# Kernel tuning notes

Hardware: AMD Instinct MI355X
Metric: run time of the kernel (lower is better)

## Reference

```python
import jax, jax.numpy as jnp
import numpy as np

T, B, D = 2048, 16, 1024


def setup_inputs() -> dict:
    key = jax.random.key(0)
    ks = jax.random.split(key, 8)
    std = 1.0 / D ** 0.5
    x = jax.random.normal(ks[0], (T, B, D), dtype=jnp.float32)
    h0 = jnp.zeros((B, D), dtype=jnp.float32)
    Wx = jax.random.uniform(ks[1], (D, D), jnp.float32, -std, std)
    R = jax.random.uniform(ks[2], (D, D), jnp.float32, -std, std)
    bias = jnp.zeros((D,), dtype=jnp.float32)
    W_delta = jax.random.uniform(ks[3], (D, D), jnp.float32, -std * 0.1, std * 0.1)
    b_delta = jnp.full((D,), 3.0, dtype=jnp.float32)  # delta_init
    A = jax.random.uniform(ks[4], (D,), jnp.float32, -0.5, 0.5)  # A_init_range
    W_gate_x = jax.random.uniform(ks[5], (D, D), jnp.float32, -std, std)
    W_gate_h = jax.random.uniform(ks[6], (D, D), jnp.float32, -std, std)
    b_gate = jnp.zeros((D,), dtype=jnp.float32)
    return {"x": x, "h0": h0, "Wx": Wx, "R": R, "bias": bias,
            "W_delta": W_delta, "b_delta": b_delta, "A": A,
            "W_gate_x": W_gate_x, "W_gate_h": W_gate_h, "b_gate": b_gate}


def reference(x, h0, Wx, R, bias, W_delta, b_delta, A, W_gate_x, W_gate_h, b_gate):
    # Input-dependent timestep: dt = softplus(x @ W_delta^T + b_delta), [T,B,D]
    dt = jax.nn.softplus(jnp.einsum('tbd,ed->tbe', x, W_delta) + b_delta)
    # Mamba-style log parameterization: decay_rate in (0,1), alpha in (0,1)
    decay_rate = jnp.exp(-jnp.exp(A))                 # [D]
    alpha = jnp.exp(-dt * decay_rate)                 # [T,B,D]
    # Precompute input projection once (big GEMM outside the scan)
    wx = jnp.einsum('tbd,ed->tbe', x, Wx) + bias      # [T,B,D]

    def step(h, inp):
        wx_t, a_t = inp                               # [B,D], [B,D]
        cand = jnp.tanh(h @ R.T + wx_t)               # nonlinear candidate
        h_new = a_t * h + (1.0 - a_t) * cand          # exponential blend
        return h_new, h_new

    _, h_out = jax.lax.scan(step, h0, (wx, alpha))    # h_out: [T,B,D] == h[1:]

    # h+x selective output gate
    gate_raw = (jnp.einsum('tbd,ed->tbe', x, W_gate_x)
                + jnp.einsum('tbd,ed->tbe', h_out, W_gate_h) + b_gate)
    return h_out * jax.nn.silu(gate_raw)
```

## Files before the change

### kernel.cpp

```cpp
#include <hip/hip_runtime.h>
#include <cstdint>
#include <cstddef>

typedef _Float16 f16;
typedef _Float16 f16x8 __attribute__((ext_vector_type(8)));
typedef _Float16 f16x4v __attribute__((ext_vector_type(4)));
typedef float f32x4 __attribute__((ext_vector_type(4)));
typedef unsigned uint2v __attribute__((ext_vector_type(2)));

#define TT 2048
#define BB 16
#define DD 1024
#define MM (TT*BB)
#define LDST 40
#define FPAD 16

__global__ void cvt_kernel(const float* __restrict__ in, f16* __restrict__ out, int n4){
  int stride = gridDim.x * blockDim.x;
  for (int j = blockIdx.x*blockDim.x + threadIdx.x; j < n4; j += stride){
    float4 v = ((const float4*)in)[j];
    f16x4v o;
    o[0]=(f16)v.x; o[1]=(f16)v.y; o[2]=(f16)v.z; o[3]=(f16)v.w;
    ((f16x4v*)out)[j] = o;
  }
}

__global__ void init_rec_kernel(const float* __restrict__ h0, f16* __restrict__ hbuf,
                                unsigned* __restrict__ flags){
  int tid = blockIdx.x*blockDim.x + threadIdx.x;
  if (tid < 64*FPAD) flags[tid] = 0u;
  if (tid < BB*DD) hbuf[tid] = (f16)h0[tid];
}

__global__ __launch_bounds__(256)
void gemm_f16_kernel(const f16* __restrict__ A, const f16* __restrict__ Bw,
                     float* __restrict__ out32, f16* __restrict__ out16,
                     const float* __restrict__ vec1, const float* __restrict__ vec2,
                     const f16* __restrict__ gxin, int epi)
{
  __shared__ f16 As[128*LDST];
  __shared__ f16 Bs[128*LDST];
  const int K = DD;
  int tid = threadIdx.x;
  int l = tid & 63, w = tid >> 6;
  int wr = w >> 1, wc = w & 1;
  int bm = blockIdx.x, bn = blockIdx.y;

  f32x4 acc[4][4];
  #pragma unroll
  for (int i=0;i<4;++i)
    #pragma unroll
    for (int j=0;j<4;++j)
      acc[i][j] = (f32x4){0.f,0.f,0.f,0.f};

  const int r0 = tid >> 2;
  const int q  = tid & 3;

  for (int kt = 0; kt < K/32; ++kt){
    __syncthreads();
    #pragma unroll
    for (int hh=0; hh<2; ++hh){
      int row = hh*64 + r0;
      uint4 va = *(const uint4*)(A  + (size_t)(bm*128+row)*K + kt*32 + q*8);
      uint4 vb = *(const uint4*)(Bw + (size_t)(bn*128+row)*K + kt*32 + q*8);
      *(uint4*)(As + row*LDST + q*8) = va;
      *(uint4*)(Bs + row*LDST + q*8) = vb;
    }
    __syncthreads();
    int lr = l & 15, kg = (l >> 4) * 8;
    f16x8 af[4], bf[4];
    #pragma unroll
    for (int i=0;i<4;++i){
      af[i] = *(const f16x8*)(As + (wr*64 + i*16 + lr)*LDST + kg);
      bf[i] = *(const f16x8*)(Bs + (wc*64 + i*16 + lr)*LDST + kg);
    }
    #pragma unroll
    for (int i=0;i<4;++i)
      #pragma unroll
      for (int j=0;j<4;++j)
        acc[i][j] = __builtin_amdgcn_mfma_f32_16x16x32_f16(af[i], bf[j], acc[i][j], 0,0,0);
  }

  int lr = l & 15, lh = l >> 4;
  #pragma unroll
  for (int i=0;i<4;++i){
    #pragma unroll
    for (int j=0;j<4;++j){
      #pragma unroll
      for (int r=0;r<4;++r){
        int row = bm*128 + wr*64 + i*16 + lh*4 + r;
        int col = bn*128 + wc*64 + j*16 + lr;
        float v = acc[i][j][r];
        size_t off = (size_t)row*DD + col;
        if (epi == 0){
          out32[off] = v + vec1[col];
        } else if (epi == 1){
          float pre = v + vec1[col];
          float sp  = (pre > 20.f) ? pre : log1pf(expf(pre));
          float decay = expf(-expf(vec2[col]));
          out32[off] = expf(-sp*decay);
        } else if (epi == 2){
          out16[off] = (f16)(v + vec1[col]);
        } else {
          float g = v + (float)gxin[off];
          float hval = (float)A[off];
          out32[off] = hval * g / (1.f + expf(-g));
        }
      }
    }
  }
}

__global__ __launch_bounds__(256)
void rec_kernel(const f16* __restrict__ Rf, const float* __restrict__ wx,
                const float* __restrict__ alpha, const float* __restrict__ h0,
                f16* __restrict__ hbuf, f16* __restrict__ hout,
                unsigned* __restrict__ flags)
{
  __shared__ f16  Rlds[32*64*8];
  __shared__ float plds[3*64*4];

  int tid = threadIdx.x;
  int l = tid & 63, w = tid >> 6;
  int j = blockIdx.x;
  int e0 = j * 16;

  for (int it=0; it<8; ++it){
    int c = it*256 + tid;
    int lane = c & 63, kt = c >> 6;
    int e = e0 + (lane & 15);
    int d = kt*32 + (lane >> 4)*8;
    uint4 v = *(const uint4*)(Rf + (size_t)e*DD + d);
    *(uint4*)(Rlds + (size_t)c*8) = v;
  }

  int b = l & 15, rr0 = (l >> 4) * 4;
  float4 hstate = {0.f,0.f,0.f,0.f};
  if (w == 0)
    hstate = *(const float4*)(h0 + (size_t)b*DD + e0 + rr0);
  __syncthreads();

  for (int t = 0; t < TT; ++t){
    f32x4 wxv, alv;
    size_t off4 = ((size_t)t*BB + b)*DD + e0 + rr0;
    if (w == 0){
      if (t > 0){
        const unsigned* fp = flags + l*FPAD;
        int guard = 0;
        unsigned long long notready = 1ull;
        while (notready && guard < 1000000){
          unsigned fv = __hip_atomic_load(fp, __ATOMIC_RELAXED, __HIP_MEMORY_SCOPE_AGENT);
          notready = __ballot(fv < (unsigned)t);
          ++guard;
          if (notready) __builtin_amdgcn_s_sleep(1);
        }
      }
      wxv = *(const f32x4*)(wx + off4);
      alv = *(const f32x4*)(alpha + off4);
    } else {
      wxv = (f32x4){0,0,0,0};
      alv = (f32x4){0,0,0,0};
    }
    __syncthreads();

    const f16* hb = hbuf + (size_t)(t & 1) * (BB*DD);
    f16x8 bfrag[8];
    #pragma unroll
    for (int kk=0; kk<8; ++kk){
      int kt = w*8 + kk;
      const f16* hp = hb + (size_t)(l & 15)*DD + kt*32 + ((l >> 4)*8);
      asm volatile("global_load_dwordx4 %0, %1, off sc0 sc1"
                   : "=v"(bfrag[kk]) : "v"(hp) : "memory");
    }
    asm volatile("s_waitcnt vmcnt(0)" ::: "memory");
    __builtin_amdgcn_sched_barrier(0);

    f32x4 acc = (f32x4){0.f,0.f,0.f,0.f};
    #pragma unroll
    for (int kk=0; kk<8; ++kk){
      int kt = w*8 + kk;
      f16x8 a = *(const f16x8*)(Rlds + ((size_t)kt*64 + l)*8);
      acc = __builtin_amdgcn_mfma_f32_16x16x32_f16(a, bfrag[kk], acc, 0, 0, 0);
    }
    if (w) *(f32x4*)(plds + ((size_t)(w-1)*64 + l)*4) = acc;
    __syncthreads();

    if (w == 0){
      f32x4 v = acc;
      #pragma unroll
      for (int q=0;q<3;++q)
        v += *(const f32x4*)(plds + ((size_t)q*64 + l)*4);

      f16x4v h4;
      float hs[4] = {hstate.x, hstate.y, hstate.z, hstate.w};
      #pragma unroll
      for (int r=0;r<4;++r){
        float z = v[r] + wxv[r];
        float cand = tanhf(z);
        float hn = alv[r]*hs[r] + (1.f - alv[r])*cand;
        hs[r] = hn;
        h4[r] = (f16)hn;
      }
      hstate = (float4){hs[0], hs[1], hs[2], hs[3]};

      f16* hw = hbuf + (size_t)((t+1) & 1) * (BB*DD) + (size_t)b*DD + e0 + rr0;
      uint2v hv = __builtin_bit_cast(uint2v, h4);
      asm volatile("global_store_dwordx2 %0, %1, off sc0 sc1"
                   :: "v"(hw), "v"(hv) : "memory");
      asm volatile("s_waitcnt vmcnt(0)" ::: "memory");
      if (l == 0)
        __hip_atomic_store(flags + j*FPAD, (unsigned)(t+1),
                           __ATOMIC_RELAXED, __HIP_MEMORY_SCOPE_AGENT);
      *(f16x4v*)(hout + off4) = h4;
    }
  }
}

extern "C" void kernel_launch(void* const* d_in, const int* in_sizes, int n_in,
                              void* d_out, int out_size, void* d_ws, size_t ws_size,
                              hipStream_t stream)
{
  const float* x    = (const float*)d_in[0];
  const float* h0   = (const float*)d_in[1];
  const float* Wx   = (const float*)d_in[2];
  const float* R    = (const float*)d_in[3];
  const float* bias = (const float*)d_in[4];
  const float* Wd   = (const float*)d_in[5];
  const float* bd   = (const float*)d_in[6];
  const float* Aar  = (const float*)d_in[7];
  const float* Wgx  = (const float*)d_in[8];
  const float* Wgh  = (const float*)d_in[9];
  const float* bg   = (const float*)d_in[10];
  float* out = (float*)d_out;

  char* ws = (char*)d_ws;
  size_t off = 0;
  auto carve = [&](size_t bytes) -> void* {
    void* p = ws + off;
    off += (bytes + 255) & ~(size_t)255;
    return p;
  };
  f16* x16    = (f16*)carve((size_t)MM*DD*2);
  f16* Wx16   = (f16*)carve((size_t)DD*DD*2);
  f16* Wd16   = (f16*)carve((size_t)DD*DD*2);
  f16* Wgx16  = (f16*)carve((size_t)DD*DD*2);
  f16* Wgh16  = (f16*)carve((size_t)DD*DD*2);
  f16* R16    = (f16*)carve((size_t)DD*DD*2);
  float* alphaB = (float*)carve((size_t)MM*DD*4);
  f16* gx16   = (f16*)carve((size_t)MM*DD*2);
  f16* hout16 = (f16*)carve((size_t)MM*DD*2);
  f16* hbuf   = (f16*)carve((size_t)2*BB*DD*2);
  unsigned* flags = (unsigned*)carve(64*FPAD*4);
  if (off > ws_size) return;

  float* wxbuf = out;

  cvt_kernel<<<1024, 256, 0, stream>>>(x,   x16,   MM*DD/4);
  cvt_kernel<<<256,  256, 0, stream>>>(Wx,  Wx16,  DD*DD/4);
  cvt_kernel<<<256,  256, 0, stream>>>(Wd,  Wd16,  DD*DD/4);
  cvt_kernel<<<256,  256, 0, stream>>>(Wgx, Wgx16, DD*DD/4);
  cvt_kernel<<<256,  256, 0, stream>>>(Wgh, Wgh16, DD*DD/4);
  cvt_kernel<<<256,  256, 0, stream>>>(R,   R16,   DD*DD/4);
  init_rec_kernel<<<64, 256, 0, stream>>>(h0, hbuf, flags);

  dim3 gg(MM/128, DD/128);
  gemm_f16_kernel<<<gg, 256, 0, stream>>>(x16, Wx16,  wxbuf,  nullptr, bias, nullptr, nullptr, 0);
  gemm_f16_kernel<<<gg, 256, 0, stream>>>(x16, Wd16,  alphaB, nullptr, bd,   Aar,     nullptr, 1);
  gemm_f16_kernel<<<gg, 256, 0, stream>>>(x16, Wgx16, nullptr, gx16,   bg,   nullptr, nullptr, 2);

  rec_kernel<<<64, 256, 0, stream>>>(R16, wxbuf, alphaB, h0, hbuf, hout16, flags);

  gemm_f16_kernel<<<gg, 256, 0, stream>>>(hout16, Wgh16, out, nullptr, nullptr, nullptr, gx16, 3);
}
```

Baseline: 8.055 ms.

## Replace flag-based inter-block sync with sequence-tagged hidden-state records

The recurrent kernel previously had one wavefront spin on per-block flags, then do a block barrier, then all waves load the hidden state. Now every wave polls the hidden-state data directly. Each 4-element f16 chunk is packed into a 16-byte record that carries its timestep tag, and a wave retries its loads until all tags match. This removes the separate store-wait-then-flag-store handshake and the pre-load barrier on the serial critical path. In exchange, the hidden-state traffic per step doubles, and correctness depends on each 16-byte store landing atomically.

```diff
diff --git a/kernel.cpp b/kernel.cpp
--- a/kernel.cpp
+++ b/kernel.cpp
@@ -7,13 +7,14 @@
 typedef _Float16 f16x4v __attribute__((ext_vector_type(4)));
 typedef float f32x4 __attribute__((ext_vector_type(4)));
 typedef unsigned uint2v __attribute__((ext_vector_type(2)));
+typedef unsigned uint4v __attribute__((ext_vector_type(4)));
 
 #define TT 2048
 #define BB 16
 #define DD 1024
 #define MM (TT*BB)
 #define LDST 40
-#define FPAD 16
+#define NREC (BB*DD/4)
 
 __global__ void cvt_kernel(const float* __restrict__ in, f16* __restrict__ out, int n4){
   int stride = gridDim.x * blockDim.x;
@@ -25,11 +26,17 @@
   }
 }
 
-__global__ void init_rec_kernel(const float* __restrict__ h0, f16* __restrict__ hbuf,
-                                unsigned* __restrict__ flags){
+__global__ void init_rec_kernel(const float* __restrict__ h0, uint4v* __restrict__ recs){
   int tid = blockIdx.x*blockDim.x + threadIdx.x;
-  if (tid < 64*FPAD) flags[tid] = 0u;
-  if (tid < BB*DD) hbuf[tid] = (f16)h0[tid];
+  if (tid < NREC){
+    int b = tid >> 8, c = tid & 255;
+    float4 v = *(const float4*)(h0 + (size_t)b*DD + c*4);
+    f16x4v h4;
+    h4[0]=(f16)v.x; h4[1]=(f16)v.y; h4[2]=(f16)v.z; h4[3]=(f16)v.w;
+    uint2v hb = __builtin_bit_cast(uint2v, h4);
+    uint4v rec = {hb[0], hb[1], 0u, 0u};
+    recs[tid] = rec;
+  }
 }
 
 __global__ __launch_bounds__(256)
@@ -114,8 +121,7 @@
 __global__ __launch_bounds__(256)
 void rec_kernel(const f16* __restrict__ Rf, const float* __restrict__ wx,
                 const float* __restrict__ alpha, const float* __restrict__ h0,
-                f16* __restrict__ hbuf, f16* __restrict__ hout,
-                unsigned* __restrict__ flags)
+                uint4v* __restrict__ recs, f16* __restrict__ hout)
 {
   __shared__ f16  Rlds[32*64*8];
   __shared__ float plds[3*64*4];
@@ -138,49 +144,50 @@
   float4 hstate = {0.f,0.f,0.f,0.f};
   if (w == 0)
     hstate = *(const float4*)(h0 + (size_t)b*DD + e0 + rr0);
+
+  const int cbase = (l & 15)*256 + (l >> 4)*2;
   __syncthreads();
 
   for (int t = 0; t < TT; ++t){
-    f32x4 wxv, alv;
+    const uint4v* rb = recs + (size_t)(t & 1) * NREC;
+    unsigned expect = (unsigned)t;
+
+    uint4v r0[8], r1[8];
+    int ok = 0;
+    for (int it = 0; it < 200000 && !ok; ++it){
+      if (it) __builtin_amdgcn_s_sleep(1);
+      #pragma unroll
+      for (int kk=0; kk<8; ++kk){
+        const uint4v* p = rb + cbase + (w*8 + kk)*8;
+        asm volatile("global_load_dwordx4 %0, %1, off sc0 sc1"
+                     : "=v"(r0[kk]) : "v"(p) : "memory");
+        asm volatile("global_load_dwordx4 %0, %1, off sc0 sc1"
+                     : "=v"(r1[kk]) : "v"(p+1) : "memory");
+      }
+      asm volatile("s_waitcnt vmcnt(0)" ::: "memory");
+      __builtin_amdgcn_sched_barrier(0);
+      unsigned bad = 0;
+      #pragma unroll
+      for (int kk=0; kk<8; ++kk)
+        bad |= (r0[kk][2] ^ expect) | (r1[kk][2] ^ expect);
+      ok = (__ballot(bad != 0) == 0ull);
+    }
+
+    f32x4 wxv = (f32x4){0,0,0,0}, alv = (f32x4){0,0,0,0};
     size_t off4 = ((size_t)t*BB + b)*DD + e0 + rr0;
     if (w == 0){
-      if (t > 0){
-        const unsigned* fp = flags + l*FPAD;
-        int guard = 0;
-        unsigned long long notready = 1ull;
-        while (notready && guard < 1000000){
-          unsigned fv = __hip_atomic_load(fp, __ATOMIC_RELAXED, __HIP_MEMORY_SCOPE_AGENT);
-          notready = __ballot(fv < (unsigned)t);
-          ++guard;
-          if (notready) __builtin_amdgcn_s_sleep(1);
-        }
-      }
       wxv = *(const f32x4*)(wx + off4);
       alv = *(const f32x4*)(alpha + off4);
-    } else {
-      wxv = (f32x4){0,0,0,0};
-      alv = (f32x4){0,0,0,0};
-    }
-    __syncthreads();
-
-    const f16* hb = hbuf + (size_t)(t & 1) * (BB*DD);
-    f16x8 bfrag[8];
+    }
+
+    f32x4 acc = (f32x4){0.f,0.f,0.f,0.f};
     #pragma unroll
     for (int kk=0; kk<8; ++kk){
       int kt = w*8 + kk;
-      const f16* hp = hb + (size_t)(l & 15)*DD + kt*32 + ((l >> 4)*8);
-      asm volatile("global_load_dwordx4 %0, %1, off sc0 sc1"
-                   : "=v"(bfrag[kk]) : "v"(hp) : "memory");
-    }
-    asm volatile("s_waitcnt vmcnt(0)" ::: "memory");
-    __builtin_amdgcn_sched_barrier(0);
-
-    f32x4 acc = (f32x4){0.f,0.f,0.f,0.f};
-    #pragma unroll
-    for (int kk=0; kk<8; ++kk){
-      int kt = w*8 + kk;
+      uint4v packed = {r0[kk][0], r0[kk][1], r1[kk][0], r1[kk][1]};
+      f16x8 bfrag = __builtin_bit_cast(f16x8, packed);
       f16x8 a = *(const f16x8*)(Rlds + ((size_t)kt*64 + l)*8);
-      acc = __builtin_amdgcn_mfma_f32_16x16x32_f16(a, bfrag[kk], acc, 0, 0, 0);
+      acc = __builtin_amdgcn_mfma_f32_16x16x32_f16(a, bfrag, acc, 0, 0, 0);
     }
     if (w) *(f32x4*)(plds + ((size_t)(w-1)*64 + l)*4) = acc;
     __syncthreads();
@@ -203,14 +210,11 @@
       }
       hstate = (float4){hs[0], hs[1], hs[2], hs[3]};
 
-      f16* hw = hbuf + (size_t)((t+1) & 1) * (BB*DD) + (size_t)b*DD + e0 + rr0;
-      uint2v hv = __builtin_bit_cast(uint2v, h4);
-      asm volatile("global_store_dwordx2 %0, %1, off sc0 sc1"
-                   :: "v"(hw), "v"(hv) : "memory");
-      asm volatile("s_waitcnt vmcnt(0)" ::: "memory");
-      if (l == 0)
-        __hip_atomic_store(flags + j*FPAD, (unsigned)(t+1),
-                           __ATOMIC_RELAXED, __HIP_MEMORY_SCOPE_AGENT);
+      uint2v hb = __builtin_bit_cast(uint2v, h4);
+      uint4v rec = {hb[0], hb[1], (unsigned)(t+1), 0u};
+      uint4v* rp = recs + (size_t)((t+1) & 1)*NREC + (size_t)b*256 + (e0 + rr0)/4;
+      asm volatile("global_store_dwordx4 %0, %1, off sc0 sc1"
+                   :: "v"(rp), "v"(rec) : "memory");
       *(f16x4v*)(hout + off4) = h4;
     }
   }
@@ -249,8 +253,7 @@
   float* alphaB = (float*)carve((size_t)MM*DD*4);
   f16* gx16   = (f16*)carve((size_t)MM*DD*2);
   f16* hout16 = (f16*)carve((size_t)MM*DD*2);
-  f16* hbuf   = (f16*)carve((size_t)2*BB*DD*2);
-  unsigned* flags = (unsigned*)carve(64*FPAD*4);
+  uint4v* recs = (uint4v*)carve((size_t)2*NREC*16);
   if (off > ws_size) return;
 
   float* wxbuf = out;
@@ -261,14 +264,14 @@
   cvt_kernel<<<256,  256, 0, stream>>>(Wgx, Wgx16, DD*DD/4);
   cvt_kernel<<<256,  256, 0, stream>>>(Wgh, Wgh16, DD*DD/4);
   cvt_kernel<<<256,  256, 0, stream>>>(R,   R16,   DD*DD/4);
-  init_rec_kernel<<<64, 256, 0, stream>>>(h0, hbuf, flags);
+  init_rec_kernel<<<64, 256, 0, stream>>>(h0, recs);
 
   dim3 gg(MM/128, DD/128);
   gemm_f16_kernel<<<gg, 256, 0, stream>>>(x16, Wx16,  wxbuf,  nullptr, bias, nullptr, nullptr, 0);
   gemm_f16_kernel<<<gg, 256, 0, stream>>>(x16, Wd16,  alphaB, nullptr, bd,   Aar,     nullptr, 1);
   gemm_f16_kernel<<<gg, 256, 0, stream>>>(x16, Wgx16, nullptr, gx16,   bg,   nullptr, nullptr, 2);
 
-  rec_kernel<<<64, 256, 0, stream>>>(R16, wxbuf, alphaB, h0, hbuf, hout16, flags);
+  rec_kernel<<<64, 256, 0, stream>>>(R16, wxbuf, alphaB, h0, recs, hout16);
 
   gemm_f16_kernel<<<gg, 256, 0, stream>>>(hout16, Wgh16, out, nullptr, nullptr, nullptr, gx16, 3);
 }
```

New measurement: 11.32 ms. 1.41x slower.

## Run recurrence with one wave per block, removing intra-block barriers and LDS reduction

Applied to the files above, without the earlier changes.

The recurrent kernel now uses a single 64-lane wavefront per block that does all 32 K-tiles of the MFMA dot product itself. This removes the two per-step __syncthreads and the LDS partial-sum reduction across four waves. It also prefetches the next step's wx and alpha values so their loads overlap the current step. In exchange, each wave issues 32 serial MFMAs and 32 global loads per step instead of 8, which lengthens the per-step critical path.

```diff
diff --git a/kernel.cpp b/kernel.cpp
--- a/kernel.cpp
+++ b/kernel.cpp
@@ -111,108 +111,91 @@
   }
 }
 
-__global__ __launch_bounds__(256)
+__global__ __launch_bounds__(64)
 void rec_kernel(const f16* __restrict__ Rf, const float* __restrict__ wx,
                 const float* __restrict__ alpha, const float* __restrict__ h0,
                 f16* __restrict__ hbuf, f16* __restrict__ hout,
                 unsigned* __restrict__ flags)
 {
-  __shared__ f16  Rlds[32*64*8];
-  __shared__ float plds[3*64*4];
-
-  int tid = threadIdx.x;
-  int l = tid & 63, w = tid >> 6;
+  __shared__ f16 Rlds[32*64*8];
+
+  int l = threadIdx.x;
   int j = blockIdx.x;
   int e0 = j * 16;
 
-  for (int it=0; it<8; ++it){
-    int c = it*256 + tid;
-    int lane = c & 63, kt = c >> 6;
-    int e = e0 + (lane & 15);
-    int d = kt*32 + (lane >> 4)*8;
-    uint4 v = *(const uint4*)(Rf + (size_t)e*DD + d);
-    *(uint4*)(Rlds + (size_t)c*8) = v;
+  #pragma unroll
+  for (int kt=0; kt<32; ++kt){
+    int e = e0 + (l & 15);
+    int d = kt*32 + (l >> 4)*8;
+    *(uint4*)(Rlds + ((size_t)kt*64 + l)*8) = *(const uint4*)(Rf + (size_t)e*DD + d);
   }
 
   int b = l & 15, rr0 = (l >> 4) * 4;
-  float4 hstate = {0.f,0.f,0.f,0.f};
-  if (w == 0)
-    hstate = *(const float4*)(h0 + (size_t)b*DD + e0 + rr0);
+  float4 hstate = *(const float4*)(h0 + (size_t)b*DD + e0 + rr0);
   __syncthreads();
 
+  f32x4 wxv = *(const f32x4*)(wx + (size_t)b*DD + e0 + rr0);
+  f32x4 alv = *(const f32x4*)(alpha + (size_t)b*DD + e0 + rr0);
+
   for (int t = 0; t < TT; ++t){
-    f32x4 wxv, alv;
-    size_t off4 = ((size_t)t*BB + b)*DD + e0 + rr0;
-    if (w == 0){
-      if (t > 0){
-        const unsigned* fp = flags + l*FPAD;
-        int guard = 0;
-        unsigned long long notready = 1ull;
-        while (notready && guard < 1000000){
-          unsigned fv = __hip_atomic_load(fp, __ATOMIC_RELAXED, __HIP_MEMORY_SCOPE_AGENT);
-          notready = __ballot(fv < (unsigned)t);
-          ++guard;
-          if (notready) __builtin_amdgcn_s_sleep(1);
-        }
+    if (t > 0){
+      const unsigned* fp = flags + l*FPAD;
+      int guard = 0;
+      unsigned long long notready = 1ull;
+      while (notready && guard < 2000000){
+        unsigned fv = __hip_atomic_load(fp, __ATOMIC_RELAXED, __HIP_MEMORY_SCOPE_AGENT);
+        notready = __ballot(fv < (unsigned)t);
+        ++guard;
+        if (notready) __builtin_amdgcn_s_sleep(1);
       }
-      wxv = *(const f32x4*)(wx + off4);
-      alv = *(const f32x4*)(alpha + off4);
-    } else {
-      wxv = (f32x4){0,0,0,0};
-      alv = (f32x4){0,0,0,0};
-    }
-    __syncthreads();
+    }
 
     const f16* hb = hbuf + (size_t)(t & 1) * (BB*DD);
-    f16x8 bfrag[8];
-    #pragma unroll
-    for (int kk=0; kk<8; ++kk){
-      int kt = w*8 + kk;
-      const f16* hp = hb + (size_t)(l & 15)*DD + kt*32 + ((l >> 4)*8);
+    f16x8 hfr[32];
+    #pragma unroll
+    for (int kt=0; kt<32; ++kt){
+      const f16* hp = hb + (size_t)b*DD + kt*32 + (l >> 4)*8;
       asm volatile("global_load_dwordx4 %0, %1, off sc0 sc1"
-                   : "=v"(bfrag[kk]) : "v"(hp) : "memory");
+                   : "=v"(hfr[kt]) : "v"(hp) : "memory");
     }
     asm volatile("s_waitcnt vmcnt(0)" ::: "memory");
     __builtin_amdgcn_sched_barrier(0);
 
+    int tn = (t+1 < TT) ? (t+1) : t;
+    size_t offn = ((size_t)tn*BB + b)*DD + e0 + rr0;
+    f32x4 wxn = *(const f32x4*)(wx + offn);
+    f32x4 aln = *(const f32x4*)(alpha + offn);
+
     f32x4 acc = (f32x4){0.f,0.f,0.f,0.f};
     #pragma unroll
-    for (int kk=0; kk<8; ++kk){
-      int kt = w*8 + kk;
+    for (int kt=0; kt<32; ++kt){
       f16x8 a = *(const f16x8*)(Rlds + ((size_t)kt*64 + l)*8);
-      acc = __builtin_amdgcn_mfma_f32_16x16x32_f16(a, bfrag[kk], acc, 0, 0, 0);
-    }
-    if (w) *(f32x4*)(plds + ((size_t)(w-1)*64 + l)*4) = acc;
-    __syncthreads();
-
-    if (w == 0){
-      f32x4 v = acc;
-      #pragma unroll
-      for (int q=0;q<3;++q)
-        v += *(const f32x4*)(plds + ((size_t)q*64 + l)*4);
-
-      f16x4v h4;
-      float hs[4] = {hstate.x, hstate.y, hstate.z, hstate.w};
-      #pragma unroll
-      for (int r=0;r<4;++r){
-        float z = v[r] + wxv[r];
-        float cand = tanhf(z);
-        float hn = alv[r]*hs[r] + (1.f - alv[r])*cand;
-        hs[r] = hn;
-        h4[r] = (f16)hn;
-      }
-      hstate = (float4){hs[0], hs[1], hs[2], hs[3]};
-
-      f16* hw = hbuf + (size_t)((t+1) & 1) * (BB*DD) + (size_t)b*DD + e0 + rr0;
-      uint2v hv = __builtin_bit_cast(uint2v, h4);
-      asm volatile("global_store_dwordx2 %0, %1, off sc0 sc1"
-                   :: "v"(hw), "v"(hv) : "memory");
-      asm volatile("s_waitcnt vmcnt(0)" ::: "memory");
-      if (l == 0)
-        __hip_atomic_store(flags + j*FPAD, (unsigned)(t+1),
-                           __ATOMIC_RELAXED, __HIP_MEMORY_SCOPE_AGENT);
-      *(f16x4v*)(hout + off4) = h4;
-    }
+      acc = __builtin_amdgcn_mfma_f32_16x16x32_f16(a, hfr[kt], acc, 0, 0, 0);
+    }
+
+    f16x4v h4;
+    float hs[4] = {hstate.x, hstate.y, hstate.z, hstate.w};
+    #pragma unroll
+    for (int r=0;r<4;++r){
+      float z = acc[r] + wxv[r];
+      float cand = tanhf(z);
+      float hn = alv[r]*hs[r] + (1.f - alv[r])*cand;
+      hs[r] = hn;
+      h4[r] = (f16)hn;
+    }
+    hstate = (float4){hs[0], hs[1], hs[2], hs[3]};
+
+    f16* hw = hbuf + (size_t)((t+1) & 1) * (BB*DD) + (size_t)b*DD + e0 + rr0;
+    uint2v hv = __builtin_bit_cast(uint2v, h4);
+    asm volatile("global_store_dwordx2 %0, %1, off sc0 sc1"
+                 :: "v"(hw), "v"(hv) : "memory");
+    asm volatile("s_waitcnt vmcnt(0)" ::: "memory");
+    if (l == 0)
+      __hip_atomic_store(flags + j*FPAD, (unsigned)(t+1),
+                         __ATOMIC_RELAXED, __HIP_MEMORY_SCOPE_AGENT);
+
+    *(f16x4v*)(hout + ((size_t)t*BB + b)*DD + e0 + rr0) = h4;
+    wxv = wxn; alv = aln;
   }
 }
 
@@ -268,7 +251,7 @@
   gemm_f16_kernel<<<gg, 256, 0, stream>>>(x16, Wd16,  alphaB, nullptr, bd,   Aar,     nullptr, 1);
   gemm_f16_kernel<<<gg, 256, 0, stream>>>(x16, Wgx16, nullptr, gx16,   bg,   nullptr, nullptr, 2);
 
-  rec_kernel<<<64, 256, 0, stream>>>(R16, wxbuf, alphaB, h0, hbuf, hout16, flags);
+  rec_kernel<<<64, 64, 0, stream>>>(R16, wxbuf, alphaB, h0, hbuf, hout16, flags);
 
   gemm_f16_kernel<<<gg, 256, 0, stream>>>(hout16, Wgh16, out, nullptr, nullptr, nullptr, gx16, 3);
 }
```

Measured after the change: 7.577 ms. 5.9% less time.
